# Kernel optimization log

Measured on AMD Instinct MI355X. Metric: run time of the kernel, lower is better.

Reference implementation:

```python
import jax, jax.numpy as jnp
import numpy as np

N_NODES = 50000
N_EDGES = 800000
D = 64
N_LAYERS = 3  # zip(convs(4), batchnorms(3)) truncates to 3 executed layers
N_GRAPHS = 32
EPS_BN = 1e-5
NEG_SLOPE = 0.2


def segment_softmax(logits, seg, n):
    m = jax.ops.segment_max(logits, seg, num_segments=n)
    m = jnp.where(jnp.isfinite(m), m, 0.0)
    z = jnp.exp(logits - m[seg])
    s = jax.ops.segment_sum(z, seg, num_segments=n)
    return z / (s[seg] + 1e-16)


def setup_inputs() -> dict:
    key = jax.random.key(0)
    ks = jax.random.split(key, 16)
    s = 0.1
    return {
        "x": jax.random.normal(ks[0], (N_NODES, D), jnp.float32),
        "edge_index": jax.random.randint(ks[1], (2, N_EDGES), 0, N_NODES),
        "edge_attr": jax.random.normal(ks[2], (N_EDGES, D), jnp.float32),
        "batch": jnp.sort(jax.random.randint(ks[3], (N_NODES,), 0, N_GRAPHS)),
        # EdgeConvLayer MLP params (stacked over layers)
        "em_w1": jax.random.normal(ks[4], (N_LAYERS, 3 * D, D)) * s,
        "em_b1": jnp.zeros((N_LAYERS, D)),
        "em_w2": jax.random.normal(ks[5], (N_LAYERS, D, D)) * s,
        "em_b2": jnp.zeros((N_LAYERS, D)),
        # GATConv params (heads=1, add_self_loops=False)
        "gat_w": jax.random.normal(ks[6], (N_LAYERS, D, D)) * s,
        "att_src": jax.random.normal(ks[7], (N_LAYERS, D)) * s,
        "att_dst": jax.random.normal(ks[8], (N_LAYERS, D)) * s,
        "edge_w": jax.random.normal(ks[9], (N_LAYERS, D, D)) * s,
        "att_edge": jax.random.normal(ks[10], (N_LAYERS, D)) * s,
        "gat_bias": jnp.zeros((N_LAYERS, D)),
        # BatchNorm params
        "bn_gamma": jnp.ones((N_LAYERS, D)),
        "bn_beta": jnp.zeros((N_LAYERS, D)),
        # readout MLP
        "mlp_w1": jax.random.normal(ks[11], (D, D)) * s,
        "mlp_b1": jnp.zeros((D,)),
        "mlp_w2": jax.random.normal(ks[12], (D, D // 2)) * s,
        "mlp_b2": jnp.zeros((D // 2,)),
        "mlp_w3": jax.random.normal(ks[13], (D // 2, 1)) * s,
        "mlp_b3": jnp.zeros((1,)),
    }


def reference(x, edge_index, edge_attr, batch, em_w1, em_b1, em_w2, em_b2,
              gat_w, att_src, att_dst, edge_w, att_edge, gat_bias,
              bn_gamma, bn_beta, mlp_w1, mlp_b1, mlp_w2, mlp_b2, mlp_w3, mlp_b3):
    row, col = edge_index[0], edge_index[1]
    n = x.shape[0]
    for l in range(N_LAYERS):
        # MetaLayer edge model: cat(src, dst, edge_attr) -> 2-layer MLP
        cat = jnp.concatenate([x[row], x[col], edge_attr], axis=1)  # (E, 3D)
        eh = jax.nn.relu(cat @ em_w1[l] + em_b1[l])
        edge_attr = eh @ em_w2[l] + em_b2[l]  # (E, D)
        # GATConv, heads=1: shared linear for src/dst
        xw = x @ gat_w[l]  # (N, D)
        a_edge = edge_attr @ (edge_w[l] @ att_edge[l])  # fused lin_edge + att_edge dot
        logits = (xw @ att_src[l])[row] + (xw @ att_dst[l])[col] + a_edge
        alpha = segment_softmax(jax.nn.leaky_relu(logits, NEG_SLOPE), col, n)
        h = jax.ops.segment_sum(alpha[:, None] * xw[row], col, num_segments=n) + gat_bias[l]
        # BatchNorm (training batch stats) + ReLU
        mu = h.mean(axis=0)
        var = h.var(axis=0)
        x = jax.nn.relu((h - mu) * jax.lax.rsqrt(var + EPS_BN) * bn_gamma[l] + bn_beta[l])
    # global mean pool over graphs
    sums = jax.ops.segment_sum(x, batch, num_segments=N_GRAPHS)
    cnt = jax.ops.segment_sum(jnp.ones((n,), x.dtype), batch, num_segments=N_GRAPHS)
    g = sums / jnp.maximum(cnt, 1.0)[:, None]
    h = jax.nn.relu(g @ mlp_w1 + mlp_b1)
    h = jax.nn.relu(h @ mlp_w2 + mlp_b2)
    return h @ mlp_w3 + mlp_b3  # (N_GRAPHS, 1)
```

## Files before the change

kernel.cpp:

```cpp
#include <hip/hip_runtime.h>


#define NN 50000
#define NE 800000
#define NEG_SLOPE 0.2f

typedef __attribute__((ext_vector_type(8))) __bf16 bf16x8;
typedef __attribute__((ext_vector_type(4))) float f32x4;

__device__ __forceinline__ float4 ld4(const float* __restrict__ p){ return *(const float4* __restrict__)p; }
__device__ __forceinline__ float4 f4zero(){ return make_float4(0.f,0.f,0.f,0.f); }
__device__ __forceinline__ bf16x8 cvt8(float4 a, float4 b){
  bf16x8 r;
  r[0]=(__bf16)a.x; r[1]=(__bf16)a.y; r[2]=(__bf16)a.z; r[3]=(__bf16)a.w;
  r[4]=(__bf16)b.x; r[5]=(__bf16)b.y; r[6]=(__bf16)b.z; r[7]=(__bf16)b.w;
  return r;
}
__device__ __forceinline__ bf16x8 addpack8(bf16x8 a, bf16x8 b){
  bf16x8 r;
#pragma unroll
  for (int e = 0; e < 8; ++e) r[e] = (__bf16)((float)a[e] + (float)b[e]);
  return r;
}
__device__ __forceinline__ float4 bnrelu4(float4 v, const float* sc, const float* sh, int d){
  return make_float4(
    fmaxf(fmaf(v.x, sc[d+0], sh[d+0]), 0.f),
    fmaxf(fmaf(v.y, sc[d+1], sh[d+1]), 0.f),
    fmaxf(fmaf(v.z, sc[d+2], sh[d+2]), 0.f),
    fmaxf(fmaf(v.w, sc[d+3], sh[d+3]), 0.f));
}

__global__ __launch_bounds__(256) void setup_kernel(
    const int* __restrict__ ei_col, int* __restrict__ cnt,
    const int* __restrict__ batch, int* __restrict__ goff,
    const float* __restrict__ em_w1, const float* __restrict__ em_w2,
    const float* __restrict__ gat_w,
    const float* __restrict__ edge_w, const float* __restrict__ att_edge,
    __bf16* __restrict__ w1f, __bf16* __restrict__ w2f, __bf16* __restrict__ wnf,
    float* __restrict__ vbuf)
{
  const int b = blockIdx.x, t = threadIdx.x;
  if (b < NE/256){
    atomicAdd(&cnt[ei_col[b*256 + t]], 1);
    int n = b*256 + t;
    if (n < NN){
      int bn = batch[n];
      int bp = (n == 0) ? -1 : batch[n-1];
      for (int g = bp + 1; g <= bn; ++g) goff[g] = n;
      if (n == NN - 1){ for (int g = bn + 1; g <= 32; ++g) goff[g] = NN; }
    }
  } else {
    const int l = b - NE/256;
    const float* W1c = em_w1 + l*12288 + 8192;
    const float* W2  = em_w2 + l*4096;
    for (int p = t; p < 512; p += 256){
      int li = p & 63, ks = (p >> 6) & 1, nt = p >> 7;
      int kbase = ks*32 + (li >> 4)*8;
      int j = nt*16 + (li & 15);
      bf16x8 v1, v2;
#pragma unroll
      for (int e = 0; e < 8; ++e){
        v1[e] = (__bf16)W1c[(size_t)(kbase+e)*64 + j];
        v2[e] = (__bf16)W2[(size_t)(kbase+e)*64 + j];
      }
      *(bf16x8*)(w1f + (size_t)l*4096 + p*8) = v1;
      *(bf16x8*)(w2f + (size_t)l*4096 + p*8) = v2;
    }
    for (int pp = t; pp < 1536; pp += 256){
      int p = pp >> 9, piece = pp & 511;
      int li = piece & 63, ks = (piece >> 6) & 1, nt = piece >> 7;
      int kbase = ks*32 + (li >> 4)*8;
      int j = nt*16 + (li & 15);
      const float* W = (p == 0) ? (em_w1 + l*12288)
                     : (p == 1) ? (em_w1 + l*12288 + 4096)
                                : (gat_w + l*4096);
      bf16x8 v;
#pragma unroll
      for (int e = 0; e < 8; ++e) v[e] = (__bf16)W[(size_t)(kbase+e)*64 + j];
      *(bf16x8*)(wnf + (size_t)l*12288 + (size_t)p*4096 + piece*8) = v;
    }
    if (t < 64){
      float a = 0.f;
      const float* ew = edge_w + l*4096 + t*64;
      const float* ae = att_edge + l*64;
#pragma unroll 8
      for (int j = 0; j < 64; ++j) a = fmaf(ew[j], ae[j], a);
      vbuf[l*64 + t] = a;
    }
  }
}

__global__ __launch_bounds__(256) void scanA(const int* __restrict__ cnt,
                                             int* __restrict__ soff,
                                             int* __restrict__ btot){
  __shared__ int wsum[4];
  const int b = blockIdx.x, t = threadIdx.x;
  const int lane = t & 63, w = t >> 6;
  int idx = b*256 + t;
  int v = (idx < NN) ? cnt[idx] : 0;
  int x = v;
#pragma unroll
  for (int o = 1; o < 64; o <<= 1){
    int u = __shfl_up(x, o);
    if (lane >= o) x += u;
  }
  if (lane == 63) wsum[w] = x;
  __syncthreads();
  int wo = 0;
#pragma unroll
  for (int k = 0; k < 4; ++k) if (k < w) wo += wsum[k];
  int incl = x + wo;
  if (idx < NN) soff[idx] = incl - v;
  if (t == 255) btot[b] = incl;
}
__global__ __launch_bounds__(256) void scanB(const int* __restrict__ btot,
                                             int* __restrict__ btotex,
                                             int* __restrict__ soff){
  __shared__ int wsum[4];
  const int t = threadIdx.x, lane = t & 63, w = t >> 6;
  int v = (t < 196) ? btot[t] : 0;
  int x = v;
#pragma unroll
  for (int o = 1; o < 64; o <<= 1){
    int u = __shfl_up(x, o);
    if (lane >= o) x += u;
  }
  if (lane == 63) wsum[w] = x;
  __syncthreads();
  int wo = 0;
#pragma unroll
  for (int k = 0; k < 4; ++k) if (k < w) wo += wsum[k];
  int incl = x + wo;
  if (t < 196) btotex[t] = incl - v;
  if (t == 195) soff[NN] = incl;
}
__global__ __launch_bounds__(256) void scanC(int* __restrict__ soff,
                                             const int* __restrict__ btotex){
  int idx = blockIdx.x*256 + threadIdx.x;
  if (idx < NN) soff[idx] += btotex[blockIdx.x];
}

__global__ __launch_bounds__(256) void scatter_kernel(
    const int* __restrict__ ei, const int* __restrict__ off, int* __restrict__ cur,
    int* __restrict__ srow, int* __restrict__ scol, int* __restrict__ perm){
  int e = blockIdx.x * 256 + threadIdx.x;
  int r = ei[e], c = ei[NE + e];
  int pos = off[c] + atomicAdd(&cur[c], 1);
  srow[pos] = r; scol[pos] = c; perm[pos] = e;
}

__global__ __launch_bounds__(256) void node_prep(
    const float* __restrict__ x0_in, const float* __restrict__ h_in,
    const float* __restrict__ bnpart,
    const float* __restrict__ gamma, const float* __restrict__ beta,
    const __bf16* __restrict__ wnf_l,
    const float* __restrict__ b1v,
    const float* __restrict__ asrc_g, const float* __restrict__ adst_g,
    __bf16* __restrict__ xaH, __bf16* __restrict__ xbH, __bf16* __restrict__ xwH,
    float* __restrict__ ssrc, float* __restrict__ sdst, int l)
{
  __shared__ __align__(16) __bf16 xf[64*72];
  __shared__ float sc[64], sh[64];
  __shared__ float b1s[64], asrc[64], adst[64];
  const int t = threadIdx.x;
  const int n0 = blockIdx.x * 64;
  const int w = t >> 6, lane = t & 63, m = lane & 15, kg = lane >> 4;

  if (l > 0){
    if (t < 64){
      float s = 0.f, s2 = 0.f;
#pragma unroll 8
      for (int k = 0; k < 64; ++k){
        s  += bnpart[k*128 + t];
        s2 += bnpart[k*128 + 64 + t];
      }
      float mu  = s * (1.0f / NN);
      float var = s2 * (1.0f / NN) - mu * mu;
      float iv  = rsqrtf(var + 1e-5f) * gamma[(l-1)*64 + t];
      sc[t] = iv;
      sh[t] = beta[(l-1)*64 + t] - mu * iv;
    }
    __syncthreads();
  }
  if (t < 64) b1s[t] = b1v[t];
  else if (t < 128) asrc[t-64] = asrc_g[t-64];
  else if (t < 192) adst[t-128] = adst_g[t-128];

  { const int e_loc = t >> 2, q = t & 3;
    const int n = n0 + e_loc;
    float4 v0, v1, v2, v3;
    if (n < NN){
      const float* src = ((l == 0) ? x0_in : h_in) + (size_t)n*64 + q*16;
      v0 = ld4(src); v1 = ld4(src+4); v2 = ld4(src+8); v3 = ld4(src+12);
      if (l > 0){
        v0 = bnrelu4(v0, sc, sh, q*16);
        v1 = bnrelu4(v1, sc, sh, q*16+4);
        v2 = bnrelu4(v2, sc, sh, q*16+8);
        v3 = bnrelu4(v3, sc, sh, q*16+12);
      }
    } else { v0 = v1 = v2 = v3 = f4zero(); }
    *(bf16x8*)&xf[e_loc*72 + q*16]     = cvt8(v0, v1);
    *(bf16x8*)&xf[e_loc*72 + q*16 + 8] = cvt8(v2, v3);
  }
  __syncthreads();

  const bf16x8 a0 = *(const bf16x8*)&xf[(16*w + m)*72 + kg*8];
  const bf16x8 a1 = *(const bf16x8*)&xf[(16*w + m)*72 + kg*8 + 32];
  const f32x4 z4 = {0.f, 0.f, 0.f, 0.f};

#pragma unroll
  for (int p = 0; p < 3; ++p){
    const bf16x8* Bp = (const bf16x8*)(wnf_l + (size_t)p*4096);
    f32x4 acc[4];
#pragma unroll
    for (int nt = 0; nt < 4; ++nt){
      acc[nt] = __builtin_amdgcn_mfma_f32_16x16x32_bf16(a0, Bp[(nt*2+0)*64 + lane], z4, 0, 0, 0);
      acc[nt] = __builtin_amdgcn_mfma_f32_16x16x32_bf16(a1, Bp[(nt*2+1)*64 + lane], acc[nt], 0, 0, 0);
    }
    __bf16* op = (p == 0) ? xaH : (p == 1) ? xbH : xwH;
#pragma unroll
    for (int nt = 0; nt < 4; ++nt){
      const int j = nt*16 + m;
      const float bb = (p == 0) ? b1s[j] : 0.f;
#pragma unroll
      for (int r = 0; r < 4; ++r){
        float v = acc[nt][r] + bb;
        unsigned short hu = __builtin_bit_cast(unsigned short, (__bf16)v);
        int pu = __shfl_xor((int)hu, 1);
        if (!(m & 1)){
          const int n = n0 + 16*w + 4*kg + r;
          if (n < NN){
            unsigned word = (unsigned)hu | ((unsigned)(pu & 0xffff) << 16);
            *(unsigned*)(op + (size_t)n*64 + (j & ~1)) = word;
          }
        }
      }
    }
    if (p == 2){
#pragma unroll
      for (int r = 0; r < 4; ++r){
        float s1 = 0.f, s2 = 0.f;
#pragma unroll
        for (int nt = 0; nt < 4; ++nt){
          s1 = fmaf(acc[nt][r], asrc[nt*16 + m], s1);
          s2 = fmaf(acc[nt][r], adst[nt*16 + m], s2);
        }
#pragma unroll
        for (int o = 8; o; o >>= 1){
          s1 += __shfl_xor(s1, o);
          s2 += __shfl_xor(s2, o);
        }
        if (m == 0){
          const int n = n0 + 16*w + 4*kg + r;
          if (n < NN){ ssrc[n] = s1; sdst[n] = s2; }
        }
      }
    }
  }
}

__global__ __launch_bounds__(256) void edge_mlp(
    const float* __restrict__ ea0,
    const __bf16* ea_in, __bf16* ea_out,
    const __bf16* __restrict__ xaH, const __bf16* __restrict__ xbH,
    const float* __restrict__ ssrc, const float* __restrict__ sdst,
    const int* __restrict__ srow, const int* __restrict__ scol,
    const int* __restrict__ permp,
    const __bf16* __restrict__ w1f, const __bf16* __restrict__ w2f,
    const float* __restrict__ b2v, const float* __restrict__ vv,
    float* __restrict__ lrelu, int store_ea)
{
  __shared__ __align__(16) __bf16 uvh[64*72];
  __shared__ __align__(16) unsigned ehw[2048];
  __shared__ float b2s[64], vs[64], sb[128];
  __shared__ int rs[128], cs[128], ps[128];
  const int t = threadIdx.x;
  const int w = t >> 6, l = t & 63, m = l & 15, kg = l >> 4;
  const int eb = blockIdx.x * 128;

  if (t < 128){ rs[t] = srow[eb+t]; cs[t] = scol[eb+t]; }
  else if (t < 192){ b2s[t-128] = b2v[t-128]; vs[t-128] = vv[t-128]; }
  if (permp && t < 128) ps[t] = permp[eb+t];
  __syncthreads();

  const bf16x8* B1 = (const bf16x8*)w1f;
  const bf16x8* B2 = (const bf16x8*)w2f;
  const f32x4 z4 = {0.f, 0.f, 0.f, 0.f};
  const int e_loc = t >> 2, q = t & 3;

  const int r0 = rs[e_loc],      c0 = cs[e_loc];
  const int r1 = rs[64 + e_loc], c1 = cs[64 + e_loc];
  const bf16x8* pa0 = (const bf16x8*)(xaH + (size_t)r0*64 + q*16);
  const bf16x8* pb0 = (const bf16x8*)(xbH + (size_t)c0*64 + q*16);
  const bf16x8* pa1 = (const bf16x8*)(xaH + (size_t)r1*64 + q*16);
  const bf16x8* pb1 = (const bf16x8*)(xbH + (size_t)c1*64 + q*16);
  bf16x8 g_a0l = pa0[0], g_a0h = pa0[1], g_b0l = pb0[0], g_b0h = pb0[1];
  bf16x8 g_a1l = pa1[0], g_a1h = pa1[1], g_b1l = pb1[0], g_b1h = pb1[1];
  float sb0 = 0.f, sb1 = 0.f;
  if (q == 0){ sb0 = ssrc[r0] + sdst[c0]; sb1 = ssrc[r1] + sdst[c1]; }

  bf16x8 A00, A01, A10, A11;
  { const int elA = 16*w + m;
    if (ea0){
      const float* s0 = ea0 + (size_t)ps[elA]*64 + kg*8;
      const float* s1 = ea0 + (size_t)ps[64+elA]*64 + kg*8;
      A00 = cvt8(ld4(s0),    ld4(s0+4));  A01 = cvt8(ld4(s0+32), ld4(s0+36));
      A10 = cvt8(ld4(s1),    ld4(s1+4));  A11 = cvt8(ld4(s1+32), ld4(s1+36));
    } else {
      const __bf16* s0 = ea_in + (size_t)(eb+elA)*64 + kg*8;
      const __bf16* s1 = ea_in + (size_t)(eb+64+elA)*64 + kg*8;
      A00 = *(const bf16x8*)s0;  A01 = *(const bf16x8*)(s0+32);
      A10 = *(const bf16x8*)s1;  A11 = *(const bf16x8*)(s1+32);
    }
  }

  *(bf16x8*)&uvh[e_loc*72 + q*16]     = addpack8(g_a0l, g_b0l);
  *(bf16x8*)&uvh[e_loc*72 + q*16 + 8] = addpack8(g_a0h, g_b0h);
  if (q == 0){ sb[e_loc] = sb0; sb[64 + e_loc] = sb1; }
  asm volatile("" ::: "memory");

  __bf16* esc = (__bf16*)ehw;
  auto tile_compute = [&](bf16x8 a0, bf16x8 a1, int tb){
    f32x4 acc[4];
#pragma unroll
    for (int nt = 0; nt < 4; ++nt){
      acc[nt] = __builtin_amdgcn_mfma_f32_16x16x32_bf16(a0, B1[(nt*2+0)*64 + l], z4, 0, 0, 0);
      acc[nt] = __builtin_amdgcn_mfma_f32_16x16x32_bf16(a1, B1[(nt*2+1)*64 + l], acc[nt], 0, 0, 0);
    }
#pragma unroll
    for (int nt = 0; nt < 4; ++nt){
      const int j = nt*16 + m;
#pragma unroll
      for (int r = 0; r < 4; ++r){
        const int erow = 16*w + 4*kg + r;
        float v = acc[nt][r] + (float)uvh[erow*72 + j];
        v = fmaxf(v, 0.f);
        const int piece = (w*2 + (nt>>1))*64 + (((nt&1)<<1) | (m>>3))*16 + 4*kg + r;
        esc[piece*8 + (m&7)] = (__bf16)v;
      }
    }
    asm volatile("" ::: "memory");
    bf16x8 a20 = *(const bf16x8*)(esc + (size_t)((w*2+0)*64 + kg*16 + m)*8);
    bf16x8 a21 = *(const bf16x8*)(esc + (size_t)((w*2+1)*64 + kg*16 + m)*8);
    f32x4 acc2[4];
#pragma unroll
    for (int nt = 0; nt < 4; ++nt){
      acc2[nt] = __builtin_amdgcn_mfma_f32_16x16x32_bf16(a20, B2[(nt*2+0)*64 + l], z4, 0, 0, 0);
      acc2[nt] = __builtin_amdgcn_mfma_f32_16x16x32_bf16(a21, B2[(nt*2+1)*64 + l], acc2[nt], 0, 0, 0);
    }
    float p0 = 0.f, p1 = 0.f, p2 = 0.f, p3 = 0.f;
#pragma unroll
    for (int nt = 0; nt < 4; ++nt){
      const int j = nt*16 + m;
      const float bj = b2s[j], vj = vs[j];
      float vr[4];
      vr[0] = acc2[nt][0] + bj; vr[1] = acc2[nt][1] + bj;
      vr[2] = acc2[nt][2] + bj; vr[3] = acc2[nt][3] + bj;
      if (store_ea){
        const size_t rowb = (size_t)(eb + tb + 16*w + 4*kg)*64 + (j & ~1);
#pragma unroll
        for (int r = 0; r < 4; ++r){
          unsigned short hu = __builtin_bit_cast(unsigned short, (__bf16)vr[r]);
          int pu = __shfl_xor((int)hu, 1);
          if (!(m & 1)){
            unsigned word = (unsigned)hu | ((unsigned)(pu & 0xffff) << 16);
            *(unsigned*)(ea_out + rowb + (size_t)r*64) = word;
          }
        }
      }
      p0 = fmaf(vr[0], vj, p0); p1 = fmaf(vr[1], vj, p1);
      p2 = fmaf(vr[2], vj, p2); p3 = fmaf(vr[3], vj, p3);
    }
#pragma unroll
    for (int o = 8; o; o >>= 1){
      p0 += __shfl_xor(p0, o); p1 += __shfl_xor(p1, o);
      p2 += __shfl_xor(p2, o); p3 += __shfl_xor(p3, o);
    }
    if (m == 0){
      float pv[4] = {p0, p1, p2, p3};
#pragma unroll
      for (int r = 0; r < 4; ++r){
        const int erow = 16*w + 4*kg + r;
        float logit = sb[tb + erow] + pv[r];
        lrelu[eb + tb + erow] = logit > 0.f ? logit : NEG_SLOPE * logit;
      }
    }
  };

  tile_compute(A00, A01, 0);
  asm volatile("" ::: "memory");
  *(bf16x8*)&uvh[e_loc*72 + q*16]     = addpack8(g_a1l, g_b1l);
  *(bf16x8*)&uvh[e_loc*72 + q*16 + 8] = addpack8(g_a1h, g_b1h);
  asm volatile("" ::: "memory");
  tile_compute(A10, A11, 64);
}

__global__ __launch_bounds__(256) void col_agg(
    const float* __restrict__ lrelu, const int* __restrict__ srow,
    const int* __restrict__ off, const __bf16* __restrict__ xwH,
    float* __restrict__ h)
{
  __shared__ float zS[4][128];
  __shared__ int   rS[4][128];
  const int t = threadIdx.x;
  const int lane = t & 63;
  const int wv = t >> 6;
  const int c = blockIdx.x * 4 + wv;
  const int s0 = off[c], s1 = off[c+1];
  const int L = s1 - s0;

  float l0 = (lane < L)    ? lrelu[s0+lane]    : -3.402823466e38f;
  float l1 = (lane+64 < L) ? lrelu[s0+64+lane] : -3.402823466e38f;
  int   r0 = (lane < L)    ? srow[s0+lane]     : 0;
  int   r1 = (lane+64 < L) ? srow[s0+64+lane]  : 0;

  float m = fmaxf(l0, l1);
  for (int i = lane+128; i < L; i += 64) m = fmaxf(m, lrelu[s0+i]);
#pragma unroll
  for (int o = 32; o; o >>= 1) m = fmaxf(m, __shfl_xor(m, o));

  float z0 = (lane < L)    ? expf(l0 - m) : 0.f;
  float z1 = (lane+64 < L) ? expf(l1 - m) : 0.f;
  float s = z0 + z1;
  for (int i = lane+128; i < L; i += 64) s += expf(lrelu[s0+i] - m);
#pragma unroll
  for (int o = 32; o; o >>= 1) s += __shfl_xor(s, o);
  const float inv = 1.f / (s + 1e-16f);

  zS[wv][lane] = z0;  zS[wv][64+lane] = z1;
  rS[wv][lane] = r0;  rS[wv][64+lane] = r1;
  asm volatile("" ::: "memory");

  float hv0 = 0.f, hv1 = 0.f, hv2 = 0.f, hv3 = 0.f;
  float hv4 = 0.f, hv5 = 0.f, hv6 = 0.f, hv7 = 0.f;
  if (L <= 128){
    int i = 0;
    for (; i + 8 <= L; i += 8){
      float za = zS[wv][i],   zb = zS[wv][i+1], zc = zS[wv][i+2], zd = zS[wv][i+3];
      float ze = zS[wv][i+4], zf = zS[wv][i+5], zg = zS[wv][i+6], zh = zS[wv][i+7];
      int   ra = rS[wv][i],   rb = rS[wv][i+1], rc = rS[wv][i+2], rd = rS[wv][i+3];
      int   re = rS[wv][i+4], rf = rS[wv][i+5], rg = rS[wv][i+6], rh = rS[wv][i+7];
      hv0 = fmaf(za, (float)xwH[(size_t)ra*64 + lane], hv0);
      hv1 = fmaf(zb, (float)xwH[(size_t)rb*64 + lane], hv1);
      hv2 = fmaf(zc, (float)xwH[(size_t)rc*64 + lane], hv2);
      hv3 = fmaf(zd, (float)xwH[(size_t)rd*64 + lane], hv3);
      hv4 = fmaf(ze, (float)xwH[(size_t)re*64 + lane], hv4);
      hv5 = fmaf(zf, (float)xwH[(size_t)rf*64 + lane], hv5);
      hv6 = fmaf(zg, (float)xwH[(size_t)rg*64 + lane], hv6);
      hv7 = fmaf(zh, (float)xwH[(size_t)rh*64 + lane], hv7);
    }
    for (; i < L; ++i)
      hv0 = fmaf(zS[wv][i], (float)xwH[(size_t)rS[wv][i]*64 + lane], hv0);
  } else {
    for (int i = 0; i < L; ++i){
      float z = expf(lrelu[s0+i] - m);
      int r = srow[s0+i];
      hv0 = fmaf(z, (float)xwH[(size_t)r*64 + lane], hv0);
    }
  }
  float hv = ((hv0 + hv1) + (hv2 + hv3)) + ((hv4 + hv5) + (hv6 + hv7));
  h[(size_t)c*64 + lane] = hv * inv;
}

__global__ __launch_bounds__(256) void bn_stats(
    const float* __restrict__ h, float* __restrict__ bnpart)
{
  const int g = blockIdx.x;
  const int t = threadIdx.x;
  const int d = t & 63, sub = t >> 6;
  const int n0 = g * 782;
  const int n1 = (n0 + 782 < NN) ? n0 + 782 : NN;
  float s = 0.f, s2 = 0.f;
  for (int n = n0 + sub; n < n1; n += 4){
    float v = h[(size_t)n*64 + d];
    s += v; s2 = fmaf(v, v, s2);
  }
  __shared__ float r1[4][64], r2[4][64];
  r1[sub][d] = s; r2[sub][d] = s2;
  __syncthreads();
  if (sub == 0){
    s  = r1[0][d] + r1[1][d] + r1[2][d] + r1[3][d];
    s2 = r2[0][d] + r2[1][d] + r2[2][d] + r2[3][d];
    bnpart[g*128 + d]      = s;
    bnpart[g*128 + 64 + d] = s2;
  }
}

__global__ __launch_bounds__(256) void seg_pool(
    const float* __restrict__ h, const int* __restrict__ goff,
    const float* __restrict__ bnpart,
    const float* __restrict__ gamma2, const float* __restrict__ beta2,
    float* __restrict__ pools, float* __restrict__ pcnt)
{
  __shared__ float sc[64], sh[64];
  const int g = blockIdx.x;
  const int t = threadIdx.x;
  const int d = t & 63, sub = t >> 6;
  if (t < 64){
    float s = 0.f, s2 = 0.f;
#pragma unroll 8
    for (int k = 0; k < 64; ++k){
      s  += bnpart[k*128 + t];
      s2 += bnpart[k*128 + 64 + t];
    }
    float mu  = s * (1.0f / NN);
    float var = s2 * (1.0f / NN) - mu * mu;
    float iv  = rsqrtf(var + 1e-5f) * gamma2[t];
    sc[t] = iv;
    sh[t] = beta2[t] - mu * iv;
  }
  __syncthreads();
  const int s0 = goff[g], s1 = goff[g+1];
  float s = 0.f;
  for (int n = s0 + sub; n < s1; n += 4)
    s += fmaxf(fmaf(h[(size_t)n*64 + d], sc[d], sh[d]), 0.f);
  __shared__ float r[4][64];
  r[sub][d] = s;
  __syncthreads();
  if (sub == 0){
    s = r[0][d] + r[1][d] + r[2][d] + r[3][d];
    pools[g*64 + d] = s;
    if (d == 0) pcnt[g] = (float)(s1 - s0);
  }
}

__global__ __launch_bounds__(256) void final_mlp(
    const float* __restrict__ pools, const float* __restrict__ pcnt,
    const float* __restrict__ w1, const float* __restrict__ b1,
    const float* __restrict__ w2, const float* __restrict__ b2,
    const float* __restrict__ w3, const float* __restrict__ b3,
    float* __restrict__ out)
{
  __shared__ float g[32*64], h1[32*64], h2[32*32];
  const int t = threadIdx.x;
  for (int i = t; i < 2048; i += 256) g[i] = pools[i] / fmaxf(pcnt[i >> 6], 1.0f);
  __syncthreads();
  for (int i = t; i < 2048; i += 256){
    int gi = i >> 6, d = i & 63;
    float a = b1[d];
    for (int k = 0; k < 64; ++k) a = fmaf(g[gi*64 + k], w1[k*64 + d], a);
    h1[i] = fmaxf(a, 0.f);
  }
  __syncthreads();
  for (int i = t; i < 1024; i += 256){
    int gi = i >> 5, d = i & 31;
    float a = b2[d];
    for (int k = 0; k < 64; ++k) a = fmaf(h1[gi*64 + k], w2[k*32 + d], a);
    h2[i] = fmaxf(a, 0.f);
  }
  __syncthreads();
  if (t < 32){
    float a = b3[0];
    for (int k = 0; k < 32; ++k) a = fmaf(h2[t*32 + k], w3[k], a);
    out[t] = a;
  }
}

extern "C" void kernel_launch(void* const* d_in, const int* in_sizes, int n_in,
                              void* d_out, int out_size, void* d_ws, size_t ws_size,
                              hipStream_t stream)
{
  (void)in_sizes; (void)n_in; (void)out_size; (void)ws_size;
  const float* x0       = (const float*)d_in[0];
  const int*   ei       = (const int*)  d_in[1];
  const float* ea0      = (const float*)d_in[2];
  const int*   batch    = (const int*)  d_in[3];
  const float* em_w1    = (const float*)d_in[4];
  const float* em_b1    = (const float*)d_in[5];
  const float* em_w2    = (const float*)d_in[6];
  const float* em_b2    = (const float*)d_in[7];
  const float* gat_w    = (const float*)d_in[8];
  const float* att_src  = (const float*)d_in[9];
  const float* att_dst  = (const float*)d_in[10];
  const float* edge_w   = (const float*)d_in[11];
  const float* att_edge = (const float*)d_in[12];
  const float* bn_gamma = (const float*)d_in[14];
  const float* bn_beta  = (const float*)d_in[15];
  const float* mlp_w1   = (const float*)d_in[16];
  const float* mlp_b1   = (const float*)d_in[17];
  const float* mlp_w2   = (const float*)d_in[18];
  const float* mlp_b2   = (const float*)d_in[19];
  const float* mlp_w3   = (const float*)d_in[20];
  const float* mlp_b3   = (const float*)d_in[21];
  float* out = (float*)d_out;

  const size_t N64 = (size_t)NN * 64, E64 = (size_t)NE * 64;
  float* ws    = (float*)d_ws;
  float* wsE   = ws;
  float* sxa   = wsE + E64;
  float* sxb   = sxa + N64;
  float* sxw   = sxb + N64;
  float* hbuf  = sxw + N64;
  float* bnpart= hbuf + N64;
  float* lrelu = bnpart + 64*128;
  float* pools = lrelu + NE;
  float* pcnt  = pools + 2048;
  float* ssrc  = pcnt + 32;
  float* sdst  = ssrc + NN;
  int*   cnt   = (int*)(sdst + NN);
  int*   cur   = cnt + NN;
  int*   soff  = cur + NN;
  int*   srow  = soff + NN + 1;
  int*   scol  = srow + NE;
  int*   perm  = scol + NE;
  int*   goff  = perm + NE;
  int*   btot  = goff + 40;
  int*   btotex= btot + 256;
  __bf16* eaB  = (__bf16*)wsE;
  __bf16* xaH  = (__bf16*)sxa;
  __bf16* xbH  = (__bf16*)sxb;
  __bf16* xwH  = (__bf16*)sxw;
  __bf16* w1f  = (__bf16*)(btotex + 256);
  __bf16* w2f  = w1f + 3*4096;
  __bf16* wnf  = w2f + 3*4096;
  float* vbuf  = (float*)(wnf + 3*12288);

  hipMemsetAsync(cnt, 0, 2 * NN * sizeof(int), stream);
  setup_kernel<<<NE/256 + 3, 256, 0, stream>>>(
      ei + NE, cnt, batch, goff, em_w1, em_w2, gat_w, edge_w, att_edge,
      w1f, w2f, wnf, vbuf);
  scanA<<<196, 256, 0, stream>>>(cnt, soff, btot);
  scanB<<<1, 256, 0, stream>>>(btot, btotex, soff);
  scanC<<<196, 256, 0, stream>>>(soff, btotex);
  scatter_kernel<<<NE / 256, 256, 0, stream>>>(ei, soff, cur, srow, scol, perm);

  for (int l = 0; l < 3; ++l){
    node_prep<<<(NN + 63) / 64, 256, 0, stream>>>(
        x0, hbuf, bnpart, bn_gamma, bn_beta,
        wnf + (size_t)l*12288, em_b1 + l*64, att_src + l*64, att_dst + l*64,
        xaH, xbH, xwH, ssrc, sdst, l);

    edge_mlp<<<NE / 128, 256, 0, stream>>>(
        (l == 0) ? ea0 : nullptr, eaB, eaB, xaH, xbH, ssrc, sdst,
        srow, scol, (l == 0) ? perm : nullptr,
        w1f + (size_t)l*4096, w2f + (size_t)l*4096,
        em_b2 + l*64, vbuf + l*64, lrelu, (l < 2) ? 1 : 0);

    col_agg<<<NN / 4, 256, 0, stream>>>(lrelu, srow, soff, xwH, hbuf);

    bn_stats<<<64, 256, 0, stream>>>(hbuf, bnpart);
  }

  seg_pool<<<32, 256, 0, stream>>>(hbuf, goff, bnpart,
                                   bn_gamma + 128, bn_beta + 128, pools, pcnt);
  final_mlp<<<1, 256, 0, stream>>>(pools, pcnt, mlp_w1, mlp_b1, mlp_w2, mlp_b2,
                                   mlp_w3, mlp_b3, out);
}
```

Before: 749.4 us.

## Process 256 edges per edge_mlp block with software-pipelined tile gathers

```diff
diff --git a/kernel.cpp b/kernel.cpp
--- a/kernel.cpp
+++ b/kernel.cpp
@@ -272,54 +272,51 @@
 {
   __shared__ __align__(16) __bf16 uvh[64*72];
   __shared__ __align__(16) unsigned ehw[2048];
-  __shared__ float b2s[64], vs[64], sb[128];
-  __shared__ int rs[128], cs[128], ps[128];
+  __shared__ float b2s[64], vs[64], sb[256];
+  __shared__ int rs[256], cs[256], ps[256];
   const int t = threadIdx.x;
   const int w = t >> 6, l = t & 63, m = l & 15, kg = l >> 4;
-  const int eb = blockIdx.x * 128;
-
-  if (t < 128){ rs[t] = srow[eb+t]; cs[t] = scol[eb+t]; }
-  else if (t < 192){ b2s[t-128] = b2v[t-128]; vs[t-128] = vv[t-128]; }
-  if (permp && t < 128) ps[t] = permp[eb+t];
+  const int eb = blockIdx.x * 256;
+
+  rs[t] = srow[eb+t]; cs[t] = scol[eb+t];
+  if (permp) ps[t] = permp[eb+t];
+  if (t < 64) b2s[t] = b2v[t];
+  else if (t < 128) vs[t-64] = vv[t-64];
   __syncthreads();
 
   const bf16x8* B1 = (const bf16x8*)w1f;
   const bf16x8* B2 = (const bf16x8*)w2f;
   const f32x4 z4 = {0.f, 0.f, 0.f, 0.f};
   const int e_loc = t >> 2, q = t & 3;
-
-  const int r0 = rs[e_loc],      c0 = cs[e_loc];
-  const int r1 = rs[64 + e_loc], c1 = cs[64 + e_loc];
-  const bf16x8* pa0 = (const bf16x8*)(xaH + (size_t)r0*64 + q*16);
-  const bf16x8* pb0 = (const bf16x8*)(xbH + (size_t)c0*64 + q*16);
-  const bf16x8* pa1 = (const bf16x8*)(xaH + (size_t)r1*64 + q*16);
-  const bf16x8* pb1 = (const bf16x8*)(xbH + (size_t)c1*64 + q*16);
-  bf16x8 g_a0l = pa0[0], g_a0h = pa0[1], g_b0l = pb0[0], g_b0h = pb0[1];
-  bf16x8 g_a1l = pa1[0], g_a1h = pa1[1], g_b1l = pb1[0], g_b1h = pb1[1];
-  float sb0 = 0.f, sb1 = 0.f;
-  if (q == 0){ sb0 = ssrc[r0] + sdst[c0]; sb1 = ssrc[r1] + sdst[c1]; }
-
-  bf16x8 A00, A01, A10, A11;
-  { const int elA = 16*w + m;
-    if (ea0){
-      const float* s0 = ea0 + (size_t)ps[elA]*64 + kg*8;
-      const float* s1 = ea0 + (size_t)ps[64+elA]*64 + kg*8;
-      A00 = cvt8(ld4(s0),    ld4(s0+4));  A01 = cvt8(ld4(s0+32), ld4(s0+36));
-      A10 = cvt8(ld4(s1),    ld4(s1+4));  A11 = cvt8(ld4(s1+32), ld4(s1+36));
-    } else {
-      const __bf16* s0 = ea_in + (size_t)(eb+elA)*64 + kg*8;
-      const __bf16* s1 = ea_in + (size_t)(eb+64+elA)*64 + kg*8;
-      A00 = *(const bf16x8*)s0;  A01 = *(const bf16x8*)(s0+32);
-      A10 = *(const bf16x8*)s1;  A11 = *(const bf16x8*)(s1+32);
-    }
-  }
-
-  *(bf16x8*)&uvh[e_loc*72 + q*16]     = addpack8(g_a0l, g_b0l);
-  *(bf16x8*)&uvh[e_loc*72 + q*16 + 8] = addpack8(g_a0h, g_b0h);
-  if (q == 0){ sb[e_loc] = sb0; sb[64 + e_loc] = sb1; }
-  asm volatile("" ::: "memory");
-
+  const int elA = 16*w + m;
   __bf16* esc = (__bf16*)ehw;
+
+  bf16x8 al0,ah0,bl0,bh0,A00,A01;
+  bf16x8 al1,ah1,bl1,bh1,A10,A11;
+  bf16x8 al2,ah2,bl2,bh2,A20,A21;
+  bf16x8 al3,ah3,bl3,bh3,A30,A31;
+
+#define LOAD_TILE(K) do{                                                      \
+    const int rK = rs[K*64 + e_loc], cK = cs[K*64 + e_loc];                   \
+    const bf16x8* pa = (const bf16x8*)(xaH + (size_t)rK*64 + q*16);           \
+    const bf16x8* pb = (const bf16x8*)(xbH + (size_t)cK*64 + q*16);           \
+    al##K = pa[0]; ah##K = pa[1]; bl##K = pb[0]; bh##K = pb[1];               \
+    if (q == 0) sb[K*64 + e_loc] = ssrc[rK] + sdst[cK];                       \
+    if (ea0){                                                                 \
+      const float* s = ea0 + (size_t)ps[K*64 + elA]*64 + kg*8;                \
+      A##K##0 = cvt8(ld4(s), ld4(s+4)); A##K##1 = cvt8(ld4(s+32), ld4(s+36)); \
+    } else {                                                                  \
+      const __bf16* s = ea_in + (size_t)(eb + K*64 + elA)*64 + kg*8;          \
+      A##K##0 = *(const bf16x8*)s; A##K##1 = *(const bf16x8*)(s+32);          \
+    }                                                                         \
+  }while(0)
+
+#define UVW_TILE(K) do{                                                       \
+    *(bf16x8*)&uvh[e_loc*72 + q*16]     = addpack8(al##K, bl##K);             \
+    *(bf16x8*)&uvh[e_loc*72 + q*16 + 8] = addpack8(ah##K, bh##K);             \
+    asm volatile("" ::: "memory");                                            \
+  }while(0)
+
   auto tile_compute = [&](bf16x8 a0, bf16x8 a1, int tb){
     f32x4 acc[4];
 #pragma unroll
@@ -385,14 +382,16 @@
         lrelu[eb + tb + erow] = logit > 0.f ? logit : NEG_SLOPE * logit;
       }
     }
+    asm volatile("" ::: "memory");
   };
 
-  tile_compute(A00, A01, 0);
-  asm volatile("" ::: "memory");
-  *(bf16x8*)&uvh[e_loc*72 + q*16]     = addpack8(g_a1l, g_b1l);
-  *(bf16x8*)&uvh[e_loc*72 + q*16 + 8] = addpack8(g_a1h, g_b1h);
-  asm volatile("" ::: "memory");
-  tile_compute(A10, A11, 64);
+  LOAD_TILE(0); LOAD_TILE(1);
+  UVW_TILE(0); LOAD_TILE(2); tile_compute(A00, A01, 0);
+  UVW_TILE(1); LOAD_TILE(3); tile_compute(A10, A11, 64);
+  UVW_TILE(2);               tile_compute(A20, A21, 128);
+  UVW_TILE(3);               tile_compute(A30, A31, 192);
+#undef LOAD_TILE
+#undef UVW_TILE
 }
 
 __global__ __launch_bounds__(256) void col_agg(
@@ -630,7 +629,7 @@
         wnf + (size_t)l*12288, em_b1 + l*64, att_src + l*64, att_dst + l*64,
         xaH, xbH, xwH, ssrc, sdst, l);
 
-    edge_mlp<<<NE / 128, 256, 0, stream>>>(
+    edge_mlp<<<NE / 256, 256, 0, stream>>>(
         (l == 0) ? ea0 : nullptr, eaB, eaB, xaH, xbH, ssrc, sdst,
         srow, scol, (l == 0) ? perm : nullptr,
         w1f + (size_t)l*4096, w2f + (size_t)l*4096,
```

Result: slower. 830.2 us (+10.8%).
